# Kernel tuning notes

Hardware: AMD Instinct MI355X
Metric: run time of the kernel (lower is better)

The kernel has to match this reference:

```python
import jax, jax.numpy as jnp
import numpy as np

M, N, RANK = 4096, 4096, 64
LORA_ALPHA = 0.8
CODEBOOK_SCALE = 1.03  # E8P12 opt_scale; decompressed weights are divided by it


def fwht(x):
    """Normalized fast Walsh-Hadamard transform along the last axis (power-of-2 length).
    Matches matmul_hadU for power-of-2 dims (had_K is None, K=1)."""
    n = x.shape[-1]
    orig = x.shape
    x = x.reshape(-1, n)
    h = 1
    while h < n:
        x = x.reshape(-1, n // (2 * h), 2, h)
        a, b = x[:, :, 0, :], x[:, :, 1, :]
        x = jnp.stack([a + b, a - b], axis=2).reshape(-1, n)
        h *= 2
    return (x / jnp.sqrt(jnp.float32(n))).reshape(orig)


def decode_e8p(codes, grid):
    """E8P lattice codebook dequant (decompress_packed_e8p semantics).
    codes: int32 [M, N//8], one 16-bit codeword per 8-weight group.
    grid:  int32 [256] packed abs codebook; 8 nibbles per entry, nibble = 2*|w| in {1,3,5,7}.
    Bit layout: [0:8]=abs grid index, [8:15]=signs of first 7 coords,
    [15]=global +/-0.25 shift. 8th sign keeps the negative-sign count even."""
    abs_idx = codes & 0xFF
    sign_bits = (codes >> 8) & 0x7F
    shift_bit = (codes >> 15) & 1
    packed = grid[abs_idx]                                      # [M, N//8] int32
    nibs = (packed[..., None] >> (4 * jnp.arange(8))) & 0xF     # [M, N//8, 8]
    s7 = 1.0 - 2.0 * ((sign_bits[..., None] >> jnp.arange(7)) & 1).astype(jnp.float32)
    s8 = jnp.prod(s7, axis=-1, keepdims=True)                   # parity sign for 8th coord
    signs = jnp.concatenate([s7, s8], axis=-1)                  # [M, N//8, 8]
    delta = (2.0 * shift_bit.astype(jnp.float32) - 1.0)[..., None] * 0.25
    w = signs * (0.5 * nibs.astype(jnp.float32)) + delta
    return w.reshape(codes.shape[0], -1) / CODEBOOK_SCALE       # [M, N]


def build_W(Qidxs, grid, SU, SV, Wscale):
    W = decode_e8p(Qidxs, grid)   # [M, N]
    W = fwht(W)                   # Hadamard over in_features
    W = fwht(W.T).T               # Hadamard over out_features
    # per-channel sign/scale rescale; SV absorbs the global Wscale (SV *= Wscale)
    return W * (SV * Wscale)[:, None] * SU[None, :]


def setup_inputs() -> dict:
    key = jax.random.key(0)
    k1, k2, k3, k4, k5 = jax.random.split(key, 5)
    rng = np.random.default_rng(0)
    # packed abs codebook: 8 nibbles per int32, nibble = 2*|w| in {1,3,5,7}
    nibs = rng.integers(0, 4, size=(256, 8)).astype(np.int64) * 2 + 1
    grid = (nibs * (1 << (4 * np.arange(8)))).sum(axis=1).astype(np.int32)
    # one random 16-bit codeword per 8-weight group (int64 packing pre-split to int32)
    codes = rng.integers(0, 2 ** 16, size=(M, N // 8)).astype(np.int32)
    return {
        "input": jax.random.normal(k1, (1, 1024, N), dtype=jnp.float32),
        "SU": jnp.where(jax.random.uniform(k2, (N,)) < 0.5, -1.0, 1.0).astype(jnp.float32),
        "SV": jnp.where(jax.random.uniform(k3, (M,)) < 0.5, -1.0, 1.0).astype(jnp.float32),
        "Wscale": jnp.float32(0.02),
        "lora_A": jax.random.normal(k4, (M, RANK), dtype=jnp.float32) * 0.01,
        "lora_B": jax.random.normal(k5, (RANK, N), dtype=jnp.float32) * 0.01,
        "Qidxs": jnp.asarray(codes),
        "grid": jnp.asarray(grid),
    }


def reference(input, SU, SV, Wscale, lora_A, lora_B, Qidxs, grid):
    W = build_W(Qidxs, grid, SU, SV, Wscale)            # [M, N] dequantized weight
    out = jnp.einsum("bsn,mn->bsm", input, W)           # base quantized matmul
    lr = jnp.einsum("bsn,rn->bsr", input, lora_B)       # low-rank path
    out = out + LORA_ALPHA * jnp.einsum("bsr,mr->bsm", lr, lora_A)
    return out
```

## Files before the change

### kernel.cpp

```cpp
#include <hip/hip_runtime.h>
#include <hip/hip_bf16.h>

typedef unsigned short u16;
typedef float  floatx4 __attribute__((ext_vector_type(4)));
typedef short  bf16x8  __attribute__((ext_vector_type(8)));

#define GK 4352

__device__ __forceinline__ u16 f2bf_rne(float f) {
  union { float f; unsigned int u; } v; v.f = f;
  unsigned int r = v.u + 0x7FFFu + ((v.u >> 16) & 1u);
  return (u16)(r >> 16);
}
__device__ __forceinline__ float bf2f(u16 h) {
  union { unsigned int u; float f; } v; v.u = ((unsigned int)h) << 16;
  return v.f;
}

__device__ __forceinline__ void fwht4096_regs(float v[16], float* X, int w, int l) {
#pragma unroll
  for (int h = 1; h < 64; h <<= 1) {
#pragma unroll
    for (int k = 0; k < 16; ++k) {
      float o = __shfl_xor(v[k], h, 64);
      v[k] = (l & h) ? (o - v[k]) : (v[k] + o);
    }
  }
#pragma unroll
  for (int k = 0; k < 16; ++k) X[(w * 16 + k) * 64 + l] = v[k];
  __syncthreads();
  float s4 = (w & 1) ? -1.f : 1.f;
  float s5 = (w & 2) ? -1.f : 1.f;
#pragma unroll
  for (int k = 0; k < 16; ++k) {
    float x00 = X[(k     ) * 64 + l];
    float x01 = X[(k + 16) * 64 + l];
    float x10 = X[(k + 32) * 64 + l];
    float x11 = X[(k + 48) * 64 + l];
    v[k] = (x00 + s4 * x01) + s5 * (x10 + s4 * x11);
  }
#pragma unroll
  for (int h = 1; h < 16; h <<= 1) {
#pragma unroll
    for (int k = 0; k < 16; ++k) {
      if (!(k & h)) { float a = v[k], b = v[k ^ h]; v[k] = a + b; v[k ^ h] = a - b; }
    }
  }
}

__global__ void decode_kernel(const int* __restrict__ codes,
                              const int* __restrict__ grid,
                              u16* __restrict__ Wd) {
  __shared__ int sgrid[256];
  int t = threadIdx.x;
  sgrid[t] = grid[t & 255];
  __syncthreads();
  int idx = blockIdx.x * 256 + t;
  int c = codes[idx];
  int abs_idx   = c & 255;
  int sign_bits = (c >> 8) & 127;
  int dlt       = 2 * ((c >> 15) & 1) - 1;
  int packed    = sgrid[abs_idx];
  int par       = __popc(sign_bits) & 1;
  u16 w[8];
#pragma unroll
  for (int j = 0; j < 8; ++j) {
    int nib = (packed >> (4 * j)) & 15;
    int neg = (j < 7) ? ((sign_bits >> j) & 1) : par;
    int val = (neg ? -2 * nib : 2 * nib) + dlt;
    w[j] = f2bf_rne((float)val);
  }
  uint4 pk;
  pk.x = (unsigned)w[0] | ((unsigned)w[1] << 16);
  pk.y = (unsigned)w[2] | ((unsigned)w[3] << 16);
  pk.z = (unsigned)w[4] | ((unsigned)w[5] << 16);
  pk.w = (unsigned)w[6] | ((unsigned)w[7] << 16);
  int m = idx >> 9, g = idx & 511;
  ((uint4*)Wd)[(size_t)m * (GK / 8) + g] = pk;
}

__global__ __launch_bounds__(256) void prep_lora_kernel(
    const float* __restrict__ loraA, const float* __restrict__ SV,
    const float* __restrict__ WscaleP, const float* __restrict__ loraB,
    const float* __restrict__ SU, u16* __restrict__ Wd, u16* __restrict__ Bh) {
  __shared__ float X[4096];
  int r = blockIdx.x, t = threadIdx.x, l = t & 63, w = t >> 6;
  float v[16];
#pragma unroll
  for (int k = 0; k < 16; ++k) {
    int i = (w * 16 + k) * 64 + l;
    v[k] = loraA[(size_t)i * 64 + r] * SV[i];
  }
  fwht4096_regs(v, X, w, l);
  float factor = (0.8f * 263.68f / 4096.0f) / WscaleP[0];
#pragma unroll
  for (int k = 0; k < 16; ++k) {
    int i = (w * 16 + k) * 64 + l;
    Wd[(size_t)i * GK + 4096 + r] = f2bf_rne(v[k] * factor);
  }
  {
    uint4 zv = make_uint4(0, 0, 0, 0);
#pragma unroll
    for (int j = 0; j < 6; ++j) {
      int idx = t + 256 * j;
      int row = idx / 24, cs = idx % 24;
      uint4* p = (uint4*)(Wd + (size_t)(r * 64 + row) * GK + 4160) + cs;
      *p = zv;
    }
  }
  __syncthreads();
#pragma unroll
  for (int k = 0; k < 16; ++k) {
    int i = (w * 16 + k) * 64 + l;
    v[k] = loraB[(size_t)r * 4096 + i] * SU[i];
  }
  fwht4096_regs(v, X, w, l);
#pragma unroll
  for (int k = 0; k < 16; ++k) {
    int i = (w * 16 + k) * 64 + l;
    Bh[(size_t)r * 4096 + i] = f2bf_rne(v[k] * 0.015625f);
  }
}

__global__ __launch_bounds__(256) void fwht_u_kernel(const float* __restrict__ x,
                                                     const float* __restrict__ SU,
                                                     u16* __restrict__ u) {
  __shared__ float X[4096];
  int s = blockIdx.x, t = threadIdx.x, l = t & 63, w = t >> 6;
  const float* xr = x + (size_t)s * 4096;
  float v[16];
#pragma unroll
  for (int k = 0; k < 16; ++k) {
    int i = (w * 16 + k) * 64 + l;
    v[k] = xr[i] * SU[i];
  }
  fwht4096_regs(v, X, w, l);
  u16* ur = u + (size_t)s * GK;
#pragma unroll
  for (int k = 0; k < 16; ++k) {
    int i = (w * 16 + k) * 64 + l;
    ur[i] = f2bf_rne(v[k] * 0.015625f);
  }
}

__device__ __forceinline__ void stage128(const u16* __restrict__ src, int rowBase,
                                         int kt, char* ldsBase, int wg, int l) {
#pragma unroll
  for (int it = 0; it < 4; ++it) {
    int ci  = it * 4 + wg;
    int row = ci * 8 + (l >> 3);
    int cg  = (l & 7) ^ ((l >> 3) & 7);
    const u16* gp = src + (size_t)(rowBase + row) * GK + kt + cg * 8;
    __builtin_amdgcn_global_load_lds(
        (const __attribute__((address_space(1))) void*)gp,
        (__attribute__((address_space(3))) void*)(ldsBase + ci * 1024), 16, 0, 0);
  }
}
__device__ __forceinline__ void stage64n(const u16* __restrict__ src,
                                         int kt, char* ldsBase, int wg, int l) {
#pragma unroll
  for (int it = 0; it < 2; ++it) {
    int ci  = it * 4 + wg;
    int row = ci * 8 + (l >> 3);
    int cg  = (l & 7) ^ ((l >> 3) & 7);
    const u16* gp = src + (size_t)row * 4096 + kt + cg * 8;
    __builtin_amdgcn_global_load_lds(
        (const __attribute__((address_space(1))) void*)gp,
        (__attribute__((address_space(3))) void*)(ldsBase + ci * 1024), 16, 0, 0);
  }
}
__device__ __forceinline__ void stage_half(const u16* __restrict__ src, int rowBase,
                                           int kt, char* slotBase, int w, int l) {
#pragma unroll
  for (int it = 0; it < 2; ++it) {
    int ci  = it * 8 + w;
    int row = ci * 8 + (l >> 3);
    int cg  = (l & 7) ^ ((l >> 3) & 7);
    const u16* gp = src + (size_t)(rowBase + row) * GK + kt + cg * 8;
    __builtin_amdgcn_global_load_lds(
        (const __attribute__((address_space(1))) void*)gp,
        (__attribute__((address_space(3))) void*)(slotBase + ci * 1024), 16, 0, 0);
  }
}

__global__ __launch_bounds__(256) void lr_gemm_kernel(
    const u16* __restrict__ U,
    const u16* __restrict__ Bh,
    float* __restrict__ P) {
  __shared__ char lds[49152];
  int t = threadIdx.x, w = t >> 6, l = t & 63;
  int s0 = blockIdx.x * 128, k0 = blockIdx.y * 1024;
  int lr16 = l & 15, lk = l >> 4;
  char* ldsA = lds;
  char* ldsB = lds + 32768;

  floatx4 acc[2][4];
#pragma unroll
  for (int i = 0; i < 2; ++i)
#pragma unroll
    for (int j = 0; j < 4; ++j) acc[i][j] = (floatx4){0.f, 0.f, 0.f, 0.f};

  const int NT = 16;
  stage128(U,  s0, k0,      ldsA,         w, l);
  stage64n(Bh,     k0,      ldsB,         w, l);
  stage128(U,  s0, k0 + 64, ldsA + 16384, w, l);
  stage64n(Bh,     k0 + 64, ldsB + 8192,  w, l);
  asm volatile("s_waitcnt vmcnt(6)" ::: "memory");
  __builtin_amdgcn_s_barrier();

  for (int i = 0; i < NT; ++i) {
    int buf = i & 1;
    const char* sAc = ldsA + buf * 16384;
    const char* sBc = ldsB + buf * 8192;
    bf16x8 a[2][2], b[4][2];
#pragma unroll
    for (int ii = 0; ii < 2; ++ii)
#pragma unroll
      for (int ks = 0; ks < 2; ++ks) {
        int row = w * 32 + ii * 16 + lr16;
        int kb  = ks * 64 + lk * 16;
        a[ii][ks] = *(const bf16x8*)(sAc + (row << 7) + (kb ^ ((row & 7) << 4)));
      }
#pragma unroll
    for (int jj = 0; jj < 4; ++jj)
#pragma unroll
      for (int ks = 0; ks < 2; ++ks) {
        int row = jj * 16 + lr16;
        int kb  = ks * 64 + lk * 16;
        b[jj][ks] = *(const bf16x8*)(sBc + (row << 7) + (kb ^ ((row & 7) << 4)));
      }
    asm volatile("s_waitcnt lgkmcnt(0)" ::: "memory");
    __builtin_amdgcn_sched_barrier(0);
    bool do_stage = (i + 2) < NT;
    if (do_stage) {
      __builtin_amdgcn_s_barrier();
      stage128(U,  s0, k0 + (i + 2) * 64, ldsA + buf * 16384, w, l);
      stage64n(Bh,     k0 + (i + 2) * 64, ldsB + buf * 8192,  w, l);
    }
#pragma unroll
    for (int ks = 0; ks < 2; ++ks)
#pragma unroll
      for (int ii = 0; ii < 2; ++ii)
#pragma unroll
        for (int jj = 0; jj < 4; ++jj)
          acc[ii][jj] = __builtin_amdgcn_mfma_f32_16x16x32_bf16(
              a[ii][ks], b[jj][ks], acc[ii][jj], 0, 0, 0);
    if (i + 1 < NT) {
      if (do_stage) asm volatile("s_waitcnt vmcnt(6)" ::: "memory");
      else          asm volatile("s_waitcnt vmcnt(0)" ::: "memory");
      __builtin_amdgcn_s_barrier();
    }
  }
  float* Pb = P + (size_t)blockIdx.y * 65536;
#pragma unroll
  for (int ii = 0; ii < 2; ++ii)
#pragma unroll
    for (int jj = 0; jj < 4; ++jj) {
      int col  = jj * 16 + lr16;
      int rowb = s0 + w * 32 + ii * 16 + lk * 4;
#pragma unroll
      for (int q = 0; q < 4; ++q)
        Pb[(size_t)(rowb + q) * 64 + col] = acc[ii][jj][q];
    }
}

__global__ void lr_reduce_kernel(const float* __restrict__ P, u16* __restrict__ u) {
  int idx = blockIdx.x * 256 + threadIdx.x;
  float s = P[idx] + P[65536 + idx] + P[131072 + idx] + P[196608 + idx];
  int ss = idx >> 6, rr = idx & 63;
  u16* row = u + (size_t)ss * GK;
  row[4096 + rr] = f2bf_rne(s);
  row[4160 + rr] = 0;
  row[4224 + rr] = 0;
  row[4288 + rr] = 0;
}

__device__ __forceinline__ void rda(bf16x8 (&dst)[4][2], const char* base, int roff,
                                    int lr16, int lk) {
#pragma unroll
  for (int ii = 0; ii < 4; ++ii)
#pragma unroll
    for (int ks = 0; ks < 2; ++ks) {
      int r = roff + ii * 16 + lr16;
      dst[ii][ks] = *(const bf16x8*)(base + (r << 7) +
          ((ks * 64 + lk * 16) ^ ((r & 7) << 4)));
    }
}
__device__ __forceinline__ void rdb(bf16x8 (&dst)[2][2], const char* base, int roff,
                                    int lr16, int lk) {
#pragma unroll
  for (int jj = 0; jj < 2; ++jj)
#pragma unroll
    for (int ks = 0; ks < 2; ++ks) {
      int r = roff + jj * 16 + lr16;
      dst[jj][ks] = *(const bf16x8*)(base + (r << 7) +
          ((ks * 64 + lk * 16) ^ ((r & 7) << 4)));
    }
}
template<int IO, int JO>
__device__ __forceinline__ void mfq(const bf16x8 (&af)[4][2], const bf16x8 (&bf)[2][2],
                                    floatx4 (&acc)[8][4]) {
  __builtin_amdgcn_s_setprio(1);
#pragma unroll
  for (int ks = 0; ks < 2; ++ks)
#pragma unroll
    for (int ii = 0; ii < 4; ++ii)
#pragma unroll
      for (int jj = 0; jj < 2; ++jj)
        acc[IO + ii][JO + jj] = __builtin_amdgcn_mfma_f32_16x16x32_bf16(
            af[ii][ks], bf[jj][ks], acc[IO + ii][JO + jj], 0, 0, 0);
  __builtin_amdgcn_s_setprio(0);
}
#define PH_PRE()  do { __builtin_amdgcn_s_barrier(); \
                       asm volatile("s_waitcnt lgkmcnt(0)" ::: "memory"); } while (0)
#define PH_POST() __builtin_amdgcn_s_barrier()

__global__ __launch_bounds__(512, 2) void gemm_kernel(
    const u16* __restrict__ A,
    const u16* __restrict__ Bm,
    u16* __restrict__ zO,
    u16* __restrict__ zW) {
  __shared__ char lds[131072];
  int t = threadIdx.x, w = t >> 6, l = t & 63;
  int b = blockIdx.x;
  int xcd = b & 7, slot = b >> 3;
  int cell = slot >> 4, j4 = slot & 15;
  int x = (xcd & 3) * 4 + (j4 & 3);
  int g = (xcd >> 2) + 2 * cell;
  int y = j4 >> 2;
  int m0 = x * 256, s0 = y * 256;
  int wsd = w >> 2, wmd = w & 3;
  int lr16 = l & 15, lk = l >> 4;
  int boff = (wmd & 1) * 64;

  const char* A0b = lds + wsd * 16384;
  const char* B0b = lds + 32768 + (wmd >> 1) * 16384;
  const char* A1b = lds + 65536 + wsd * 16384;
  const char* B1b = lds + 98304 + (wmd >> 1) * 16384;

  floatx4 acc[8][4];
#pragma unroll
  for (int i = 0; i < 8; ++i)
#pragma unroll
    for (int jq = 0; jq < 4; ++jq) acc[i][jq] = (floatx4){0.f, 0.f, 0.f, 0.f};

  int kb0 = g * 1088;

  stage_half(A,  s0,       kb0,      lds +      0, w, l);
  stage_half(A,  s0 + 128, kb0,      lds +  16384, w, l);
  stage_half(Bm, m0,       kb0,      lds +  32768, w, l);
  stage_half(Bm, m0 + 128, kb0,      lds +  49152, w, l);
  stage_half(Bm, m0,       kb0 + 64, lds +  98304, w, l);
  stage_half(Bm, m0 + 128, kb0 + 64, lds + 114688, w, l);
  asm volatile("s_waitcnt vmcnt(4)" ::: "memory");
  __builtin_amdgcn_s_barrier();

  for (int j = 0; j < 8; ++j) {
    int kt1  = kb0 + (2 * j + 1) * 64;
    int ktn0 = kb0 + (2 * j + 2) * 64;
    int ktn1 = kb0 + (2 * j + 3) * 64;
    bf16x8 aF[4][2], aG[4][2], bF[2][2], bG[2][2];
    rda(aF, A0b, 0, lr16, lk); rdb(bF, B0b, boff, lr16, lk);
    stage_half(A, s0, kt1, lds + 65536, w, l);
    PH_PRE(); mfq<0, 0>(aF, bF, acc); PH_POST();
    rdb(bG, B0b, boff + 32, lr16, lk);
    stage_half(A, s0 + 128, kt1, lds + 81920, w, l);
    PH_PRE(); mfq<0, 2>(aF, bG, acc); PH_POST();
    rda(aG, A0b, 64, lr16, lk);
    stage_half(Bm, m0, ktn0, lds + 32768, w, l);
    PH_PRE(); mfq<4, 0>(aG, bF, acc); PH_POST();
    stage_half(Bm, m0 + 128, ktn0, lds + 49152, w, l);
    PH_PRE(); mfq<4, 2>(aG, bG, acc);
    asm volatile("s_waitcnt vmcnt(4)" ::: "memory");
    PH_POST();
    rda(aF, A1b, 0, lr16, lk); rdb(bF, B1b, boff, lr16, lk);
    stage_half(A, s0, ktn0, lds + 0, w, l);
    PH_PRE(); mfq<0, 0>(aF, bF, acc); PH_POST();
    rdb(bG, B1b, boff + 32, lr16, lk);
    stage_half(A, s0 + 128, ktn0, lds + 16384, w, l);
    PH_PRE(); mfq<0, 2>(aF, bG, acc); PH_POST();
    rda(aG, A1b, 64, lr16, lk);
    if (j < 7) stage_half(Bm, m0, ktn1, lds + 98304, w, l);
    PH_PRE(); mfq<4, 0>(aG, bF, acc); PH_POST();
    if (j < 7) stage_half(Bm, m0 + 128, ktn1, lds + 114688, w, l);
    PH_PRE(); mfq<4, 2>(aG, bG, acc);
    asm volatile("s_waitcnt vmcnt(4)" ::: "memory");
    PH_POST();
  }
  asm volatile("s_waitcnt vmcnt(0)" ::: "memory");
  __builtin_amdgcn_s_barrier();
  {
    bf16x8 aF[4][2], aG[4][2], bF[2][2], bG[2][2];
    rda(aF, A0b, 0, lr16, lk); rdb(bF, B0b, boff, lr16, lk);
    PH_PRE(); mfq<0, 0>(aF, bF, acc); PH_POST();
    rdb(bG, B0b, boff + 32, lr16, lk);
    PH_PRE(); mfq<0, 2>(aF, bG, acc); PH_POST();
    rda(aG, A0b, 64, lr16, lk);
    PH_PRE(); mfq<4, 0>(aG, bF, acc); PH_POST();
    PH_PRE(); mfq<4, 2>(aG, bG, acc);
  }
  u16* dst = (g < 2) ? zO : zW;
  int gg = g & 1;
#pragma unroll
  for (int ii = 0; ii < 8; ++ii)
#pragma unroll
    for (int jj = 0; jj < 4; ++jj) {
      int col  = m0 + wmd * 64 + jj * 16 + lr16;
      int rowb = s0 + wsd * 128 + ii * 16 + lk * 4;
#pragma unroll
      for (int q = 0; q < 4; ++q)
        dst[(size_t)(rowb + q) * 8192 + gg * 4096 + col] = f2bf_rne(acc[ii][jj][q]);
    }
}

__global__ __launch_bounds__(256) void final_kernel(const float* __restrict__ SV,
                                                    const float* __restrict__ WscaleP,
                                                    const u16* __restrict__ zW,
                                                    float* __restrict__ out) {
  __shared__ float X[4096];
  int s = blockIdx.x, t = threadIdx.x, l = t & 63, w = t >> 6;
  const u16* zr = (const u16*)out + (size_t)s * 8192;
  const u16* zw = zW + (size_t)s * 8192;
  float v[16];
#pragma unroll
  for (int k = 0; k < 16; ++k) {
    int i = (w * 16 + k) * 64 + l;
    v[k] = (bf2f(zr[i]) + bf2f(zr[4096 + i])) + (bf2f(zw[i]) + bf2f(zw[4096 + i]));
  }
  fwht4096_regs(v, X, w, l);
  float gscale = WscaleP[0] * (1.0f / 263.68f);
  float* orow = out + (size_t)s * 4096;
#pragma unroll
  for (int k = 0; k < 16; ++k) {
    int i = (w * 16 + k) * 64 + l;
    orow[i] = v[k] * gscale * SV[i];
  }
}

extern "C" void kernel_launch(void* const* d_in, const int* in_sizes, int n_in,
                              void* d_out, int out_size, void* d_ws, size_t ws_size,
                              hipStream_t stream) {
  const float* x      = (const float*)d_in[0];
  const float* SU     = (const float*)d_in[1];
  const float* SV     = (const float*)d_in[2];
  const float* Wscale = (const float*)d_in[3];
  const float* loraA  = (const float*)d_in[4];
  const float* loraB  = (const float*)d_in[5];
  const int*   Qidxs  = (const int*)d_in[6];
  const int*   grid   = (const int*)d_in[7];
  float* out = (float*)d_out;

  char* ws = (char*)d_ws;
  u16* Wd = (u16*)ws;
  u16* u  = (u16*)(ws + 35651584);
  u16* Bh = (u16*)(ws + 35651584 + 8912896);
  float* P = (float*)(ws + 35651584 + 8912896 + 524288);
  u16* zW = (u16*)(ws + 35651584 + 8912896 + 524288 + 1048576);
  u16* zO = (u16*)out;

  decode_kernel<<<8192, 256, 0, stream>>>(Qidxs, grid, Wd);
  prep_lora_kernel<<<64, 256, 0, stream>>>(loraA, SV, Wscale, loraB, SU, Wd, Bh);
  fwht_u_kernel<<<1024, 256, 0, stream>>>(x, SU, u);
  dim3 lg(8, 4);
  lr_gemm_kernel<<<lg, 256, 0, stream>>>(u, Bh, P);
  lr_reduce_kernel<<<256, 256, 0, stream>>>(P, u);
  gemm_kernel<<<256, 512, 0, stream>>>(u, Wd, zO, zW);
  final_kernel<<<1024, 256, 0, stream>>>(SV, Wscale, zW, out);
}
```

Baseline: 94.54 us.

## Merge decode, LoRA prep and input FWHT into one launch; vectorize bf16 I/O

Replaces the three preprocessing kernels (E8P decode, LoRA factor transforms, input Hadamard) with a single kernel whose blocks branch on blockIdx, removing two launches and their serialization gaps. The input FWHT output is staged through LDS so the bf16 row is written with 16-byte stores. The final kernel also loads the bf16 partial sums with 16-byte vector loads into LDS before the transform. The changes add extra LDS traffic and barriers, and block-role branching creates heterogeneous block durations.

```diff
diff --git a/kernel.cpp b/kernel.cpp
--- a/kernel.cpp
+++ b/kernel.cpp
@@ -48,98 +48,100 @@
   }
 }
 
-__global__ void decode_kernel(const int* __restrict__ codes,
-                              const int* __restrict__ grid,
-                              u16* __restrict__ Wd) {
-  __shared__ int sgrid[256];
-  int t = threadIdx.x;
-  sgrid[t] = grid[t & 255];
-  __syncthreads();
-  int idx = blockIdx.x * 256 + t;
-  int c = codes[idx];
-  int abs_idx   = c & 255;
-  int sign_bits = (c >> 8) & 127;
-  int dlt       = 2 * ((c >> 15) & 1) - 1;
-  int packed    = sgrid[abs_idx];
-  int par       = __popc(sign_bits) & 1;
-  u16 w[8];
-#pragma unroll
-  for (int j = 0; j < 8; ++j) {
-    int nib = (packed >> (4 * j)) & 15;
-    int neg = (j < 7) ? ((sign_bits >> j) & 1) : par;
-    int val = (neg ? -2 * nib : 2 * nib) + dlt;
-    w[j] = f2bf_rne((float)val);
-  }
-  uint4 pk;
-  pk.x = (unsigned)w[0] | ((unsigned)w[1] << 16);
-  pk.y = (unsigned)w[2] | ((unsigned)w[3] << 16);
-  pk.z = (unsigned)w[4] | ((unsigned)w[5] << 16);
-  pk.w = (unsigned)w[6] | ((unsigned)w[7] << 16);
-  int m = idx >> 9, g = idx & 511;
-  ((uint4*)Wd)[(size_t)m * (GK / 8) + g] = pk;
-}
-
-__global__ __launch_bounds__(256) void prep_lora_kernel(
-    const float* __restrict__ loraA, const float* __restrict__ SV,
-    const float* __restrict__ WscaleP, const float* __restrict__ loraB,
-    const float* __restrict__ SU, u16* __restrict__ Wd, u16* __restrict__ Bh) {
+__global__ __launch_bounds__(256) void prep_all_kernel(
+    const float* __restrict__ x, const float* __restrict__ SU,
+    const float* __restrict__ SV, const float* __restrict__ WscaleP,
+    const float* __restrict__ loraA, const float* __restrict__ loraB,
+    const int* __restrict__ codes, const int* __restrict__ grid,
+    u16* __restrict__ Wd, u16* __restrict__ u, u16* __restrict__ Bh) {
   __shared__ float X[4096];
-  int r = blockIdx.x, t = threadIdx.x, l = t & 63, w = t >> 6;
-  float v[16];
-#pragma unroll
-  for (int k = 0; k < 16; ++k) {
-    int i = (w * 16 + k) * 64 + l;
-    v[k] = loraA[(size_t)i * 64 + r] * SV[i];
-  }
-  fwht4096_regs(v, X, w, l);
-  float factor = (0.8f * 263.68f / 4096.0f) / WscaleP[0];
-#pragma unroll
-  for (int k = 0; k < 16; ++k) {
-    int i = (w * 16 + k) * 64 + l;
-    Wd[(size_t)i * GK + 4096 + r] = f2bf_rne(v[k] * factor);
-  }
-  {
-    uint4 zv = make_uint4(0, 0, 0, 0);
-#pragma unroll
-    for (int j = 0; j < 6; ++j) {
-      int idx = t + 256 * j;
-      int row = idx / 24, cs = idx % 24;
-      uint4* p = (uint4*)(Wd + (size_t)(r * 64 + row) * GK + 4160) + cs;
-      *p = zv;
-    }
-  }
-  __syncthreads();
-#pragma unroll
-  for (int k = 0; k < 16; ++k) {
-    int i = (w * 16 + k) * 64 + l;
-    v[k] = loraB[(size_t)r * 4096 + i] * SU[i];
-  }
-  fwht4096_regs(v, X, w, l);
-#pragma unroll
-  for (int k = 0; k < 16; ++k) {
-    int i = (w * 16 + k) * 64 + l;
-    Bh[(size_t)r * 4096 + i] = f2bf_rne(v[k] * 0.015625f);
-  }
-}
-
-__global__ __launch_bounds__(256) void fwht_u_kernel(const float* __restrict__ x,
-                                                     const float* __restrict__ SU,
-                                                     u16* __restrict__ u) {
-  __shared__ float X[4096];
-  int s = blockIdx.x, t = threadIdx.x, l = t & 63, w = t >> 6;
-  const float* xr = x + (size_t)s * 4096;
-  float v[16];
-#pragma unroll
-  for (int k = 0; k < 16; ++k) {
-    int i = (w * 16 + k) * 64 + l;
-    v[k] = xr[i] * SU[i];
-  }
-  fwht4096_regs(v, X, w, l);
-  u16* ur = u + (size_t)s * GK;
-#pragma unroll
-  for (int k = 0; k < 16; ++k) {
-    int i = (w * 16 + k) * 64 + l;
-    ur[i] = f2bf_rne(v[k] * 0.015625f);
+  int bid = blockIdx.x, t = threadIdx.x, l = t & 63, w = t >> 6;
+
+  if (bid < 1024) {
+    int s = bid;
+    const float* xr = x + (size_t)s * 4096;
+    float v[16];
+#pragma unroll
+    for (int k = 0; k < 16; ++k) {
+      int i = (w * 16 + k) * 64 + l;
+      v[k] = xr[i] * SU[i];
+    }
+    fwht4096_regs(v, X, w, l);
+    __syncthreads();
+    u16* Xu = (u16*)X;
+#pragma unroll
+    for (int k = 0; k < 16; ++k)
+      Xu[(w * 16 + k) * 64 + l] = f2bf_rne(v[k] * 0.015625f);
+    __syncthreads();
+    u16* ur = u + (size_t)s * GK;
+#pragma unroll
+    for (int c = 0; c < 2; ++c) {
+      int j = (t + 256 * c) * 8;
+      *(uint4*)(ur + j) = *(const uint4*)(Xu + j);
+    }
+  } else if (bid < 1088) {
+    int r = bid - 1024;
+    float v[16];
+#pragma unroll
+    for (int k = 0; k < 16; ++k) {
+      int i = (w * 16 + k) * 64 + l;
+      v[k] = loraA[(size_t)i * 64 + r] * SV[i];
+    }
+    fwht4096_regs(v, X, w, l);
+    float factor = (0.8f * 263.68f / 4096.0f) / WscaleP[0];
+#pragma unroll
+    for (int k = 0; k < 16; ++k) {
+      int i = (w * 16 + k) * 64 + l;
+      Wd[(size_t)i * GK + 4096 + r] = f2bf_rne(v[k] * factor);
+    }
+    {
+      uint4 zv = make_uint4(0, 0, 0, 0);
+#pragma unroll
+      for (int j = 0; j < 6; ++j) {
+        int idx = t + 256 * j;
+        int row = idx / 24, cs = idx % 24;
+        uint4* p = (uint4*)(Wd + (size_t)(r * 64 + row) * GK + 4160) + cs;
+        *p = zv;
+      }
+    }
+    __syncthreads();
+#pragma unroll
+    for (int k = 0; k < 16; ++k) {
+      int i = (w * 16 + k) * 64 + l;
+      v[k] = loraB[(size_t)r * 4096 + i] * SU[i];
+    }
+    fwht4096_regs(v, X, w, l);
+#pragma unroll
+    for (int k = 0; k < 16; ++k) {
+      int i = (w * 16 + k) * 64 + l;
+      Bh[(size_t)r * 4096 + i] = f2bf_rne(v[k] * 0.015625f);
+    }
+  } else {
+    int* sgrid = (int*)X;
+    sgrid[t] = grid[t & 255];
+    __syncthreads();
+    int idx = (bid - 1088) * 256 + t;
+    int c = codes[idx];
+    int abs_idx   = c & 255;
+    int sign_bits = (c >> 8) & 127;
+    int dlt       = 2 * ((c >> 15) & 1) - 1;
+    int packed    = sgrid[abs_idx];
+    int par       = __popc(sign_bits) & 1;
+    u16 wv[8];
+#pragma unroll
+    for (int j = 0; j < 8; ++j) {
+      int nib = (packed >> (4 * j)) & 15;
+      int neg = (j < 7) ? ((sign_bits >> j) & 1) : par;
+      int val = (neg ? -2 * nib : 2 * nib) + dlt;
+      wv[j] = f2bf_rne((float)val);
+    }
+    uint4 pk;
+    pk.x = (unsigned)wv[0] | ((unsigned)wv[1] << 16);
+    pk.y = (unsigned)wv[2] | ((unsigned)wv[3] << 16);
+    pk.z = (unsigned)wv[4] | ((unsigned)wv[5] << 16);
+    pk.w = (unsigned)wv[6] | ((unsigned)wv[7] << 16);
+    int m = idx >> 9, g = idx & 511;
+    ((uint4*)Wd)[(size_t)m * (GK / 8) + g] = pk;
   }
 }
 
@@ -421,12 +423,30 @@
   int s = blockIdx.x, t = threadIdx.x, l = t & 63, w = t >> 6;
   const u16* zr = (const u16*)out + (size_t)s * 8192;
   const u16* zw = zW + (size_t)s * 8192;
+#pragma unroll
+  for (int c = 0; c < 2; ++c) {
+    int j = (t + 256 * c) * 8;
+    uint4 a0 = *(const uint4*)(zr + j);
+    uint4 a1 = *(const uint4*)(zr + 4096 + j);
+    uint4 b0 = *(const uint4*)(zw + j);
+    uint4 b1 = *(const uint4*)(zw + 4096 + j);
+    const unsigned* pa0 = (const unsigned*)&a0;
+    const unsigned* pa1 = (const unsigned*)&a1;
+    const unsigned* pb0 = (const unsigned*)&b0;
+    const unsigned* pb1 = (const unsigned*)&b1;
+#pragma unroll
+    for (int q = 0; q < 4; ++q) {
+      X[j + 2 * q] = (bf2f((u16)pa0[q]) + bf2f((u16)pa1[q])) +
+                     (bf2f((u16)pb0[q]) + bf2f((u16)pb1[q]));
+      X[j + 2 * q + 1] = (bf2f((u16)(pa0[q] >> 16)) + bf2f((u16)(pa1[q] >> 16))) +
+                         (bf2f((u16)(pb0[q] >> 16)) + bf2f((u16)(pb1[q] >> 16)));
+    }
+  }
+  __syncthreads();
   float v[16];
 #pragma unroll
-  for (int k = 0; k < 16; ++k) {
-    int i = (w * 16 + k) * 64 + l;
-    v[k] = (bf2f(zr[i]) + bf2f(zr[4096 + i])) + (bf2f(zw[i]) + bf2f(zw[4096 + i]));
-  }
+  for (int k = 0; k < 16; ++k) v[k] = X[(w * 16 + k) * 64 + l];
+  __syncthreads();
   fwht4096_regs(v, X, w, l);
   float gscale = WscaleP[0] * (1.0f / 263.68f);
   float* orow = out + (size_t)s * 4096;
@@ -458,9 +478,8 @@
   u16* zW = (u16*)(ws + 35651584 + 8912896 + 524288 + 1048576);
   u16* zO = (u16*)out;
 
-  decode_kernel<<<8192, 256, 0, stream>>>(Qidxs, grid, Wd);
-  prep_lora_kernel<<<64, 256, 0, stream>>>(loraA, SV, Wscale, loraB, SU, Wd, Bh);
-  fwht_u_kernel<<<1024, 256, 0, stream>>>(x, SU, u);
+  prep_all_kernel<<<9280, 256, 0, stream>>>(x, SU, SV, Wscale, loraA, loraB,
+                                            Qidxs, grid, Wd, u, Bh);
   dim3 lg(8, 4);
   lr_gemm_kernel<<<lg, 256, 0, stream>>>(u, Bh, P);
   lr_reduce_kernel<<<256, 256, 0, stream>>>(P, u);
```

Result: faster. 80.56 us (-14.8%).
